# Optimization experiments

Measured on AMD Instinct MI355X. Metric: run time of the kernel, lower is better.

The kernel has to match this reference:

```python
import jax, jax.numpy as jnp
import numpy as np

B, S, D, H, DFF = 8, 1024, 1024, 16, 4096
DK = D // H
EPS = 1e-6
NEG = -1e9


def setup_inputs() -> dict:
    key = jax.random.key(0)
    ks = jax.random.split(key, 8)
    x = jax.random.normal(ks[0], (B, S, D), dtype=jnp.float32)
    mask = jnp.ones((B, 1, 1, S), dtype=jnp.int32)
    s = 0.02
    wq = jax.random.normal(ks[1], (D, D), jnp.float32) * s
    wk = jax.random.normal(ks[2], (D, D), jnp.float32) * s
    wv = jax.random.normal(ks[3], (D, D), jnp.float32) * s
    wo = jax.random.normal(ks[4], (D, D), jnp.float32) * s
    bq = jnp.zeros((D,), jnp.float32); bk = jnp.zeros((D,), jnp.float32)
    bv = jnp.zeros((D,), jnp.float32); bo = jnp.zeros((D,), jnp.float32)
    w1 = jax.random.normal(ks[5], (D, DFF), jnp.float32) * s
    b1 = jnp.zeros((DFF,), jnp.float32)
    w2 = jax.random.normal(ks[6], (DFF, D), jnp.float32) * s
    b2 = jnp.zeros((D,), jnp.float32)
    g1 = jnp.array(1.0, jnp.float32); be1 = jnp.array(0.0, jnp.float32)
    g2 = jnp.array(1.0, jnp.float32); be2 = jnp.array(0.0, jnp.float32)
    return dict(x=x, mask=mask, wq=wq, bq=bq, wk=wk, bk=bk, wv=wv, bv=bv,
                wo=wo, bo=bo, w1=w1, b1=b1, w2=w2, b2=b2,
                g1=g1, be1=be1, g2=g2, be2=be2)


def layer_norm(x, gamma, beta):
    # repo quirk: unbiased std (ddof=1), scalar gamma/beta, divide by (std+eps)
    mean = jnp.mean(x, axis=-1, keepdims=True)
    std = jnp.std(x, axis=-1, keepdims=True, ddof=1)
    return gamma * (x - mean) / (std + EPS) + beta


def mha(x, mask, wq, bq, wk, bk, wv, bv, wo, bo):
    q = (x @ wq + bq).reshape(B, S, H, DK).transpose(0, 2, 1, 3)  # bhsd
    k = (x @ wk + bk).reshape(B, S, H, DK).transpose(0, 2, 1, 3)
    v = (x @ wv + bv).reshape(B, S, H, DK).transpose(0, 2, 1, 3)
    scores = jnp.einsum('bhqd,bhkd->bhqk', q, k) / jnp.sqrt(jnp.float32(DK))
    scores = jnp.where(mask == 0, NEG, scores)
    attn = jax.nn.softmax(scores, axis=-1)
    out = jnp.einsum('bhqk,bhkd->bhqd', attn, v)
    out = out.transpose(0, 2, 1, 3).reshape(B, S, D)
    return out @ wo + bo


def reference(x, mask, wq, bq, wk, bk, wv, bv, wo, bo, w1, b1, w2, b2, g1, be1, g2, be2):
    # pre-LN residual: x + sublayer(norm(x)); dropout inert at eval
    x = x + mha(layer_norm(x, g1, be1), mask, wq, bq, wk, bk, wv, bv, wo, bo)
    h = layer_norm(x, g2, be2)
    x = x + (jax.nn.relu(h @ w1 + b1) @ w2 + b2)
    return x
```

## Files before the change

kernel.cpp:

```cpp
#include <hip/hip_runtime.h>
#include <math.h>

typedef __bf16 bf16;
typedef float f32x4 __attribute__((ext_vector_type(4)));
typedef bf16 bf16x8 __attribute__((ext_vector_type(8)));

#define DEV __device__ __forceinline__

constexpr int Ss = 1024, Dd = 1024;
constexpr float EPSf = 1e-6f;
constexpr float SM_SCALE = 0.125f * 1.4426950408889634f;

DEV void gl_lds16(const void* g, void* l) {
  __builtin_amdgcn_global_load_lds(
      (const __attribute__((address_space(1))) void*)g,
      (__attribute__((address_space(3))) void*)l, 16, 0, 0);
}

__global__ __launch_bounds__(256) void transpose6_k(
    const float* __restrict__ i0, const float* __restrict__ i1,
    const float* __restrict__ i2, const float* __restrict__ i3,
    const float* __restrict__ i4, const float* __restrict__ i5,
    bf16* __restrict__ o0, bf16* __restrict__ o1, bf16* __restrict__ o2,
    bf16* __restrict__ o3, bf16* __restrict__ o4, bf16* __restrict__ o5) {
  __shared__ float t[64 * 65];
  const int bi = blockIdx.x;
  const float* in;
  bf16* out;
  int R, C, local, sh;
  if (bi < 1024) {
    const int j = bi >> 8;
    local = bi & 255; R = 1024; C = 1024; sh = 4;
    in = (j == 0) ? i0 : (j == 1) ? i1 : (j == 2) ? i2 : i3;
    out = (j == 0) ? o0 : (j == 1) ? o1 : (j == 2) ? o2 : o3;
  } else if (bi < 2048) {
    local = bi - 1024; R = 1024; C = 4096; sh = 6; in = i4; out = o4;
  } else {
    local = bi - 2048; R = 4096; C = 1024; sh = 4; in = i5; out = o5;
  }
  const int nx = 1 << sh;
  const int bx = local & (nx - 1), by = local >> sh;
  const int tid = threadIdx.x;
  const int tx = tid & 63, ty = tid >> 6;
  const int r0 = by * 64, c0 = bx * 64;
#pragma unroll
  for (int i = 0; i < 16; i++) {
    int r = ty + i * 4;
    t[r * 65 + tx] = in[(size_t)(r0 + r) * C + c0 + tx];
  }
  __syncthreads();
#pragma unroll
  for (int i = 0; i < 16; i++) {
    int r = ty + i * 4;
    out[(size_t)(c0 + r) * R + r0 + tx] = (bf16)t[tx * 65 + r];
  }
}

__global__ __launch_bounds__(256) void transpose_b_k(
    const bf16* __restrict__ in, bf16* __restrict__ out, int ostride, int si,
    size_t isb, size_t osb) {
  __shared__ bf16 t[64 * 65];
  const int tid = threadIdx.x;
  const int tx = tid & 63, ty = tid >> 6;
  const bf16* ib = in + (size_t)blockIdx.z * isb;
  bf16* ob = out + (size_t)blockIdx.z * osb;
  const int r0 = blockIdx.y * 64, c0 = blockIdx.x * 64;
#pragma unroll
  for (int i = 0; i < 16; i++) {
    int r = ty + i * 4;
    t[r * 65 + tx] = ib[(size_t)(r0 + r) * si + c0 + tx];
  }
  __syncthreads();
#pragma unroll
  for (int i = 0; i < 16; i++) {
    int r = ty + i * 4;
    ob[(size_t)(c0 + r) * ostride + r0 + tx] = t[tx * 65 + r];
  }
}

__global__ __launch_bounds__(256) void ln_kernel(
    const float* __restrict__ in, bf16* __restrict__ out,
    const float* __restrict__ gp, const float* __restrict__ bp) {
  const int row = blockIdx.x;
  const int tid = threadIdx.x;
  float v[4];
  const float* p = in + (size_t)row * Dd + tid * 4;
#pragma unroll
  for (int i = 0; i < 4; i++) v[i] = p[i];
  float s = v[0] + v[1] + v[2] + v[3];
  float s2 = v[0] * v[0] + v[1] * v[1] + v[2] * v[2] + v[3] * v[3];
#pragma unroll
  for (int m = 1; m < 64; m <<= 1) {
    s += __shfl_xor(s, m, 64);
    s2 += __shfl_xor(s2, m, 64);
  }
  __shared__ float ls[4], ls2[4];
  if ((tid & 63) == 0) {
    ls[tid >> 6] = s;
    ls2[tid >> 6] = s2;
  }
  __syncthreads();
  s = ls[0] + ls[1] + ls[2] + ls[3];
  s2 = ls2[0] + ls2[1] + ls2[2] + ls2[3];
  float mean = s * (1.0f / Dd);
  float var = (s2 - (float)Dd * mean * mean) * (1.0f / (Dd - 1));
  var = fmaxf(var, 0.0f);
  float g = gp[0], be = bp[0];
  float rs = g / (sqrtf(var) + EPSf);
  bf16* q = out + (size_t)row * Dd + tid * 4;
#pragma unroll
  for (int i = 0; i < 4; i++) q[i] = (bf16)((v[i] - mean) * rs + be);
}

template <int EPI>
__global__ __launch_bounds__(256) void gemm_bt(
    const bf16* __restrict__ A, const bf16* __restrict__ Bt,
    const float* __restrict__ bias, const float* __restrict__ bias2,
    const float* __restrict__ bias3, const float* __restrict__ resid,
    void* __restrict__ Cout, int M, int N, int K, int sa, int sb) {
  __shared__ __attribute__((aligned(16))) bf16 As[128 * 64];
  __shared__ __attribute__((aligned(16))) bf16 Bs[128 * 64];
  const int tid = threadIdx.x;
  const int ln = tid & 63;
  const int wv = tid >> 6;
  const int wm = wv >> 1, wn = wv & 1;
  const int quad = ln >> 4, l16 = ln & 15;
  const int l7 = l16 & 7;
  const int m0 = blockIdx.y * 128, n0 = blockIdx.x * 128;

  f32x4 acc[4][4];
#pragma unroll
  for (int i = 0; i < 4; i++)
#pragma unroll
    for (int j = 0; j < 4; j++) acc[i][j] = {0.f, 0.f, 0.f, 0.f};

  const int sr = tid >> 3;
  const int sc = (tid & 7) ^ (sr & 7);
  const size_t abase = (size_t)(m0 + sr) * sa + sc * 8;
  const size_t bbase = (size_t)(n0 + sr) * sb + sc * 8;

  for (int k0 = 0; k0 < K; k0 += 64) {
#pragma unroll
    for (int j = 0; j < 4; j++) {
      gl_lds16(A + abase + (size_t)(j * 32) * sa + k0,
               (char*)As + j * 4096 + wv * 1024);
      gl_lds16(Bt + bbase + (size_t)(j * 32) * sb + k0,
               (char*)Bs + j * 4096 + wv * 1024);
    }
    __syncthreads();
#pragma unroll
    for (int kh = 0; kh < 2; kh++) {
      bf16x8 af[4], bfr[4];
#pragma unroll
      for (int mi = 0; mi < 4; mi++)
        af[mi] = *(const bf16x8*)&As[(wm * 64 + mi * 16 + l16) * 64 +
                                     ((kh * 4 + quad) ^ l7) * 8];
#pragma unroll
      for (int ni = 0; ni < 4; ni++)
        bfr[ni] = *(const bf16x8*)&Bs[(wn * 64 + ni * 16 + l16) * 64 +
                                      ((kh * 4 + quad) ^ l7) * 8];
#pragma unroll
      for (int mi = 0; mi < 4; mi++)
#pragma unroll
        for (int ni = 0; ni < 4; ni++)
          acc[mi][ni] = __builtin_amdgcn_mfma_f32_16x16x32_bf16(
              af[mi], bfr[ni], acc[mi][ni], 0, 0, 0);
    }
    __syncthreads();
  }

#pragma unroll
  for (int mi = 0; mi < 4; mi++) {
    const int m = m0 + wm * 64 + mi * 16 + quad * 4;
#pragma unroll
    for (int ni = 0; ni < 4; ni++) {
      const int n = n0 + wn * 64 + ni * 16 + l16;
      float bvl;
      if constexpr (EPI == 4) {
        const int seg = n >> 10;
        const float* bp = (seg == 0) ? bias : (seg == 1) ? bias2 : bias3;
        bvl = bp[n & 1023];
      } else if constexpr (EPI == 3) {
        bvl = 0.0f;
      } else {
        bvl = bias[n];
      }
#pragma unroll
      for (int r = 0; r < 4; r++) {
        float val = acc[mi][ni][r] + bvl;
        const size_t idx = (size_t)(m + r) * N + n;
        if constexpr (EPI == 1) {
          ((float*)Cout)[idx] = val + resid[idx];
        } else if constexpr (EPI == 2) {
          ((bf16*)Cout)[idx] = (bf16)fmaxf(val, 0.0f);
        } else if constexpr (EPI == 3) {
          ((float*)Cout)[idx] = val + resid[idx];
        } else {
          ((bf16*)Cout)[idx] = (bf16)val;
        }
      }
    }
  }
}

__global__ __launch_bounds__(256) void attn_k(
    const bf16* __restrict__ qkv, const bf16* __restrict__ vt,
    const int* __restrict__ mask, bf16* __restrict__ ctx) {
  __shared__ __attribute__((aligned(16))) bf16 Qs[128 * 64];
  __shared__ __attribute__((aligned(16))) bf16 Ks[64 * 64];
  __shared__ __attribute__((aligned(16))) bf16 Vs[64 * 64];
  __shared__ __attribute__((aligned(16))) bf16 Ps[4 * 32 * 64];
  __shared__ float Fm[1024];
  const int tid = threadIdx.x;
  const int ln = tid & 63, w = tid >> 6;
  const int quad = ln >> 4, l16 = ln & 15;
  const int l7 = l16 & 7;
  const int bh = blockIdx.y;
  const int b = bh >> 4, h = bh & 15;
  const int q0 = blockIdx.x * 128;
  const int sr = tid >> 3;
  const int sc = (tid & 7) ^ (sr & 7);

  {
    const int4 mv = *(const int4*)&mask[b * Ss + tid * 4];
    const float ninf = -__builtin_inff();
    Fm[tid * 4 + 0] = mv.x ? 0.0f : ninf;
    Fm[tid * 4 + 1] = mv.y ? 0.0f : ninf;
    Fm[tid * 4 + 2] = mv.z ? 0.0f : ninf;
    Fm[tid * 4 + 3] = mv.w ? 0.0f : ninf;
  }
  {
#pragma unroll
    for (int j = 0; j < 4; j++) {
      const size_t ga =
          (size_t)(b * Ss + q0 + j * 32 + sr) * 3072 + h * 64 + sc * 8;
      gl_lds16(qkv + ga, (char*)Qs + j * 4096 + w * 1024);
    }
  }
  __syncthreads();
  bf16x8 aq[2][2];
#pragma unroll
  for (int qi = 0; qi < 2; qi++)
#pragma unroll
    for (int c = 0; c < 2; c++)
      aq[qi][c] = *(const bf16x8*)&Qs[(w * 32 + qi * 16 + l16) * 64 +
                                      ((c * 4 + quad) ^ l7) * 8];

  f32x4 o[2][4];
#pragma unroll
  for (int qi = 0; qi < 2; qi++)
#pragma unroll
    for (int i = 0; i < 4; i++) o[qi][i] = {0.f, 0.f, 0.f, 0.f};
  f32x4 psum[2] = {{0.f, 0.f, 0.f, 0.f}, {0.f, 0.f, 0.f, 0.f}};

  for (int kk0 = 0; kk0 < Ss; kk0 += 64) {
    {
#pragma unroll
      for (int j = 0; j < 2; j++) {
        const size_t ga = (size_t)(b * Ss + kk0 + j * 32 + sr) * 3072 + 1024 +
                          h * 64 + sc * 8;
        gl_lds16(qkv + ga, (char*)Ks + j * 4096 + w * 1024);
        const size_t gv = (size_t)(bh * 64 + j * 32 + sr) * Ss + kk0 + sc * 8;
        gl_lds16(vt + gv, (char*)Vs + j * 4096 + w * 1024);
      }
    }
    __syncthreads();

    f32x4 st[2][4];
#pragma unroll
    for (int nt = 0; nt < 4; nt++) {
      bf16x8 bk0 = *(const bf16x8*)&Ks[(nt * 16 + l16) * 64 + (quad ^ l7) * 8];
      bf16x8 bk1 =
          *(const bf16x8*)&Ks[(nt * 16 + l16) * 64 + ((4 + quad) ^ l7) * 8];
#pragma unroll
      for (int qi = 0; qi < 2; qi++) {
        f32x4 s = {0.f, 0.f, 0.f, 0.f};
        s = __builtin_amdgcn_mfma_f32_16x16x32_bf16(aq[qi][0], bk0, s, 0, 0, 0);
        s = __builtin_amdgcn_mfma_f32_16x16x32_bf16(aq[qi][1], bk1, s, 0, 0, 0);
        st[qi][nt] = s;
      }
    }
    float fmv[4];
#pragma unroll
    for (int nt = 0; nt < 4; nt++) fmv[nt] = Fm[kk0 + nt * 16 + l16];
#pragma unroll
    for (int qi = 0; qi < 2; qi++)
#pragma unroll
      for (int nt = 0; nt < 4; nt++)
#pragma unroll
        for (int r = 0; r < 4; r++) {
          const float p = exp2f(fmaf(st[qi][nt][r], SM_SCALE, fmv[nt]));
          st[qi][nt][r] = p;
          psum[qi][r] += p;
        }
#pragma unroll
    for (int qi = 0; qi < 2; qi++)
#pragma unroll
      for (int nt = 0; nt < 4; nt++) {
        const int ch = nt * 2 + (l16 >> 3);
#pragma unroll
        for (int r = 0; r < 4; r++) {
          const int pr = qi * 16 + quad * 4 + r;
          Ps[w * 2048 + pr * 64 + (ch ^ (pr & 7)) * 8 + l7] =
              (bf16)st[qi][nt][r];
        }
      }
#pragma unroll
    for (int kh = 0; kh < 2; kh++) {
      bf16x8 bv[4];
#pragma unroll
      for (int dt = 0; dt < 4; dt++)
        bv[dt] = *(const bf16x8*)&Vs[(dt * 16 + l16) * 64 +
                                     ((kh * 4 + quad) ^ l7) * 8];
#pragma unroll
      for (int qi = 0; qi < 2; qi++) {
        bf16x8 ap = *(const bf16x8*)&Ps[w * 2048 + (qi * 16 + l16) * 64 +
                                        ((kh * 4 + quad) ^ l7) * 8];
#pragma unroll
        for (int dt = 0; dt < 4; dt++)
          o[qi][dt] =
              __builtin_amdgcn_mfma_f32_16x16x32_bf16(ap, bv[dt], o[qi][dt],
                                                      0, 0, 0);
      }
    }
    __syncthreads();
  }
#pragma unroll
  for (int qi = 0; qi < 2; qi++)
#pragma unroll
    for (int r = 0; r < 4; r++) {
      float s = psum[qi][r];
#pragma unroll
      for (int m = 1; m < 16; m <<= 1) s += __shfl_xor(s, m, 64);
      psum[qi][r] = s;
    }
#pragma unroll
  for (int qi = 0; qi < 2; qi++) {
    const float inv0 = 1.0f / psum[qi][0], inv1 = 1.0f / psum[qi][1];
    const float inv2 = 1.0f / psum[qi][2], inv3 = 1.0f / psum[qi][3];
#pragma unroll
    for (int dt = 0; dt < 4; dt++) {
      const size_t base =
          (size_t)(b * Ss + q0 + w * 32 + qi * 16 + quad * 4) * Dd + h * 64 +
          dt * 16 + l16;
      ctx[base] = (bf16)(o[qi][dt][0] * inv0);
      ctx[base + Dd] = (bf16)(o[qi][dt][1] * inv1);
      ctx[base + 2 * Dd] = (bf16)(o[qi][dt][2] * inv2);
      ctx[base + 3 * Dd] = (bf16)(o[qi][dt][3] * inv3);
    }
  }
}

extern "C" void kernel_launch(void* const* d_in, const int* in_sizes, int n_in,
                              void* d_out, int out_size, void* d_ws,
                              size_t ws_size, hipStream_t stream) {
  (void)in_sizes; (void)n_in; (void)out_size;
  const float* x = (const float*)d_in[0];
  const int* mask = (const int*)d_in[1];
  const float* wq = (const float*)d_in[2];
  const float* bq = (const float*)d_in[3];
  const float* wk = (const float*)d_in[4];
  const float* bk = (const float*)d_in[5];
  const float* wvw = (const float*)d_in[6];
  const float* bv = (const float*)d_in[7];
  const float* wo = (const float*)d_in[8];
  const float* bo = (const float*)d_in[9];
  const float* w1 = (const float*)d_in[10];
  const float* b1 = (const float*)d_in[11];
  const float* w2 = (const float*)d_in[12];
  const float* b2 = (const float*)d_in[13];
  const float* g1 = (const float*)d_in[14];
  const float* be1 = (const float*)d_in[15];
  const float* g2 = (const float*)d_in[16];
  const float* be2 = (const float*)d_in[17];
  float* out = (float*)d_out;

  char* ws = (char*)d_ws;
  const size_t MB = 1024 * 1024;
  bf16* w1T = (bf16*)(ws + 0 * MB);
  bf16* w2T = (bf16*)(ws + 8 * MB);
  bf16* wqkvT = (bf16*)(ws + 16 * MB);
  bf16* woT = (bf16*)(ws + 22 * MB);
  bf16* lnb = (bf16*)(ws + 24 * MB);
  bf16* qkv = (bf16*)(ws + 40 * MB);
  bf16* vtb = (bf16*)(ws + 88 * MB);
  float* x1 = (float*)(ws + 40 * MB);
  bf16* ctx = lnb;

  dim3 blk(256);
  transpose6_k<<<3072, blk, 0, stream>>>(
      wq, wk, wvw, wo, w1, w2, wqkvT, wqkvT + (size_t)1024 * 1024,
      wqkvT + (size_t)2048 * 1024, woT, w1T, w2T);
  ln_kernel<<<8192, blk, 0, stream>>>(x, lnb, g1, be1);
  gemm_bt<4><<<dim3(24, 64), blk, 0, stream>>>(
      lnb, wqkvT, bq, bk, bv, nullptr, qkv, 8192, 3072, 1024, 1024, 1024);
  transpose_b_k<<<dim3(16, 16, 8), blk, 0, stream>>>(
      qkv + 2048, vtb, 1024, 3072, (size_t)Ss * 3072, (size_t)Dd * Ss);
  attn_k<<<dim3(8, 128), blk, 0, stream>>>(qkv, vtb, mask, ctx);
  gemm_bt<1><<<dim3(8, 64), blk, 0, stream>>>(
      ctx, woT, bo, nullptr, nullptr, x, x1, 8192, 1024, 1024, 1024, 1024);
  ln_kernel<<<8192, blk, 0, stream>>>(x1, lnb, g2, be2);

  if (ws_size >= 136 * MB) {
    bf16* mid = (bf16*)(ws + 72 * MB);
    gemm_bt<2><<<dim3(32, 64), blk, 0, stream>>>(
        lnb, w1T, b1, nullptr, nullptr, nullptr, mid, 8192, 4096, 1024, 1024,
        1024);
    gemm_bt<1><<<dim3(8, 64), blk, 0, stream>>>(
        mid, w2T, b2, nullptr, nullptr, x1, out, 8192, 1024, 4096, 4096, 4096);
  } else {
    bf16* mid = (bf16*)(ws + 72 * MB);
    gemm_bt<2><<<dim3(16, 64), blk, 0, stream>>>(
        lnb, w1T, b1, nullptr, nullptr, nullptr, mid, 8192, 2048, 1024, 1024,
        1024);
    gemm_bt<1><<<dim3(8, 64), blk, 0, stream>>>(
        mid, w2T, b2, nullptr, nullptr, x1, out, 8192, 1024, 2048, 2048, 4096);
    gemm_bt<2><<<dim3(16, 64), blk, 0, stream>>>(
        lnb, w1T + (size_t)2048 * 1024, b1 + 2048, nullptr, nullptr, nullptr,
        mid, 8192, 2048, 1024, 1024, 1024);
    gemm_bt<3><<<dim3(8, 64), blk, 0, stream>>>(
        mid, w2T + 2048, nullptr, nullptr, nullptr, out, out, 8192, 1024, 2048,
        2048, 4096);
  }
}
```

Baseline: 511.2 us.

## Fuse V transpose into QKV GEMM epilogue and deepen K tile for N=1024 GEMMs

The QKV projection epilogue now writes the V third directly in transposed layout into the vtb buffer, removing the separate transpose kernel and its extra read/write of V. The GEMM is templated on the K tile size, and the output-projection and FFN-down GEMMs use a 128-wide K tile to halve loop iterations and barriers. The larger tile doubles LDS use per block, which may reduce occupancy, and the transposed V stores are narrow scattered 8-byte writes.

```diff
diff --git a/kernel.cpp b/kernel.cpp
--- a/kernel.cpp
+++ b/kernel.cpp
@@ -4,6 +4,7 @@
 typedef __bf16 bf16;
 typedef float f32x4 __attribute__((ext_vector_type(4)));
 typedef bf16 bf16x8 __attribute__((ext_vector_type(8)));
+typedef bf16 bf16x4 __attribute__((ext_vector_type(4)));
 
 #define DEV __device__ __forceinline__
 
@@ -56,28 +57,6 @@
   }
 }
 
-__global__ __launch_bounds__(256) void transpose_b_k(
-    const bf16* __restrict__ in, bf16* __restrict__ out, int ostride, int si,
-    size_t isb, size_t osb) {
-  __shared__ bf16 t[64 * 65];
-  const int tid = threadIdx.x;
-  const int tx = tid & 63, ty = tid >> 6;
-  const bf16* ib = in + (size_t)blockIdx.z * isb;
-  bf16* ob = out + (size_t)blockIdx.z * osb;
-  const int r0 = blockIdx.y * 64, c0 = blockIdx.x * 64;
-#pragma unroll
-  for (int i = 0; i < 16; i++) {
-    int r = ty + i * 4;
-    t[r * 65 + tx] = ib[(size_t)(r0 + r) * si + c0 + tx];
-  }
-  __syncthreads();
-#pragma unroll
-  for (int i = 0; i < 16; i++) {
-    int r = ty + i * 4;
-    ob[(size_t)(c0 + r) * ostride + r0 + tx] = t[tx * 65 + r];
-  }
-}
-
 __global__ __launch_bounds__(256) void ln_kernel(
     const float* __restrict__ in, bf16* __restrict__ out,
     const float* __restrict__ gp, const float* __restrict__ bp) {
@@ -112,14 +91,18 @@
   for (int i = 0; i < 4; i++) q[i] = (bf16)((v[i] - mean) * rs + be);
 }
 
-template <int EPI>
+template <int EPI, int BK>
 __global__ __launch_bounds__(256) void gemm_bt(
     const bf16* __restrict__ A, const bf16* __restrict__ Bt,
     const float* __restrict__ bias, const float* __restrict__ bias2,
     const float* __restrict__ bias3, const float* __restrict__ resid,
-    void* __restrict__ Cout, int M, int N, int K, int sa, int sb) {
-  __shared__ __attribute__((aligned(16))) bf16 As[128 * 64];
-  __shared__ __attribute__((aligned(16))) bf16 Bs[128 * 64];
+    bf16* __restrict__ vtb, void* __restrict__ Cout, int M, int N, int K,
+    int sa, int sb) {
+  __shared__ __attribute__((aligned(16))) bf16 As[128 * BK];
+  __shared__ __attribute__((aligned(16))) bf16 Bs[128 * BK];
+  constexpr int CPR = BK / 8;
+  constexpr int RPJ = 256 / CPR;
+  constexpr int NJ = BK / 16;
   const int tid = threadIdx.x;
   const int ln = tid & 63;
   const int wv = tid >> 6;
@@ -134,30 +117,30 @@
 #pragma unroll
     for (int j = 0; j < 4; j++) acc[i][j] = {0.f, 0.f, 0.f, 0.f};
 
-  const int sr = tid >> 3;
-  const int sc = (tid & 7) ^ (sr & 7);
+  const int sr = tid / CPR;
+  const int sc = (tid & (CPR - 1)) ^ (sr & 7);
   const size_t abase = (size_t)(m0 + sr) * sa + sc * 8;
   const size_t bbase = (size_t)(n0 + sr) * sb + sc * 8;
 
-  for (int k0 = 0; k0 < K; k0 += 64) {
-#pragma unroll
-    for (int j = 0; j < 4; j++) {
-      gl_lds16(A + abase + (size_t)(j * 32) * sa + k0,
+  for (int k0 = 0; k0 < K; k0 += BK) {
+#pragma unroll
+    for (int j = 0; j < NJ; j++) {
+      gl_lds16(A + abase + (size_t)(j * RPJ) * sa + k0,
                (char*)As + j * 4096 + wv * 1024);
-      gl_lds16(Bt + bbase + (size_t)(j * 32) * sb + k0,
+      gl_lds16(Bt + bbase + (size_t)(j * RPJ) * sb + k0,
                (char*)Bs + j * 4096 + wv * 1024);
     }
     __syncthreads();
 #pragma unroll
-    for (int kh = 0; kh < 2; kh++) {
+    for (int kh = 0; kh < BK / 32; kh++) {
       bf16x8 af[4], bfr[4];
 #pragma unroll
       for (int mi = 0; mi < 4; mi++)
-        af[mi] = *(const bf16x8*)&As[(wm * 64 + mi * 16 + l16) * 64 +
+        af[mi] = *(const bf16x8*)&As[(wm * 64 + mi * 16 + l16) * BK +
                                      ((kh * 4 + quad) ^ l7) * 8];
 #pragma unroll
       for (int ni = 0; ni < 4; ni++)
-        bfr[ni] = *(const bf16x8*)&Bs[(wn * 64 + ni * 16 + l16) * 64 +
+        bfr[ni] = *(const bf16x8*)&Bs[(wn * 64 + ni * 16 + l16) * BK +
                                       ((kh * 4 + quad) ^ l7) * 8];
 #pragma unroll
       for (int mi = 0; mi < 4; mi++)
@@ -185,18 +168,31 @@
       } else {
         bvl = bias[n];
       }
-#pragma unroll
-      for (int r = 0; r < 4; r++) {
-        float val = acc[mi][ni][r] + bvl;
-        const size_t idx = (size_t)(m + r) * N + n;
-        if constexpr (EPI == 1) {
-          ((float*)Cout)[idx] = val + resid[idx];
-        } else if constexpr (EPI == 2) {
-          ((bf16*)Cout)[idx] = (bf16)fmaxf(val, 0.0f);
-        } else if constexpr (EPI == 3) {
-          ((float*)Cout)[idx] = val + resid[idx];
+      if constexpr (EPI == 4) {
+        if (n < 2048) {
+#pragma unroll
+          for (int r = 0; r < 4; r++)
+            ((bf16*)Cout)[(size_t)(m + r) * N + n] =
+                (bf16)(acc[mi][ni][r] + bvl);
         } else {
-          ((bf16*)Cout)[idx] = (bf16)val;
+          bf16x4 tv;
+#pragma unroll
+          for (int r = 0; r < 4; r++) tv[r] = (bf16)(acc[mi][ni][r] + bvl);
+          const size_t vrow = (size_t)((m >> 10) * 1024 + (n - 2048));
+          *(bf16x4*)&vtb[vrow * Ss + (m & 1023)] = tv;
+        }
+      } else {
+#pragma unroll
+        for (int r = 0; r < 4; r++) {
+          float val = acc[mi][ni][r] + bvl;
+          const size_t idx = (size_t)(m + r) * N + n;
+          if constexpr (EPI == 1) {
+            ((float*)Cout)[idx] = val + resid[idx];
+          } else if constexpr (EPI == 2) {
+            ((bf16*)Cout)[idx] = (bf16)fmaxf(val, 0.0f);
+          } else {
+            ((float*)Cout)[idx] = val + resid[idx];
+          }
         }
       }
     }
@@ -392,34 +388,35 @@
       wq, wk, wvw, wo, w1, w2, wqkvT, wqkvT + (size_t)1024 * 1024,
       wqkvT + (size_t)2048 * 1024, woT, w1T, w2T);
   ln_kernel<<<8192, blk, 0, stream>>>(x, lnb, g1, be1);
-  gemm_bt<4><<<dim3(24, 64), blk, 0, stream>>>(
-      lnb, wqkvT, bq, bk, bv, nullptr, qkv, 8192, 3072, 1024, 1024, 1024);
-  transpose_b_k<<<dim3(16, 16, 8), blk, 0, stream>>>(
-      qkv + 2048, vtb, 1024, 3072, (size_t)Ss * 3072, (size_t)Dd * Ss);
+  gemm_bt<4, 64><<<dim3(24, 64), blk, 0, stream>>>(
+      lnb, wqkvT, bq, bk, bv, nullptr, vtb, qkv, 8192, 3072, 1024, 1024, 1024);
   attn_k<<<dim3(8, 128), blk, 0, stream>>>(qkv, vtb, mask, ctx);
-  gemm_bt<1><<<dim3(8, 64), blk, 0, stream>>>(
-      ctx, woT, bo, nullptr, nullptr, x, x1, 8192, 1024, 1024, 1024, 1024);
+  gemm_bt<1, 128><<<dim3(8, 64), blk, 0, stream>>>(
+      ctx, woT, bo, nullptr, nullptr, x, nullptr, x1, 8192, 1024, 1024, 1024,
+      1024);
   ln_kernel<<<8192, blk, 0, stream>>>(x1, lnb, g2, be2);
 
   if (ws_size >= 136 * MB) {
     bf16* mid = (bf16*)(ws + 72 * MB);
-    gemm_bt<2><<<dim3(32, 64), blk, 0, stream>>>(
-        lnb, w1T, b1, nullptr, nullptr, nullptr, mid, 8192, 4096, 1024, 1024,
-        1024);
-    gemm_bt<1><<<dim3(8, 64), blk, 0, stream>>>(
-        mid, w2T, b2, nullptr, nullptr, x1, out, 8192, 1024, 4096, 4096, 4096);
+    gemm_bt<2, 64><<<dim3(32, 64), blk, 0, stream>>>(
+        lnb, w1T, b1, nullptr, nullptr, nullptr, nullptr, mid, 8192, 4096,
+        1024, 1024, 1024);
+    gemm_bt<1, 128><<<dim3(8, 64), blk, 0, stream>>>(
+        mid, w2T, b2, nullptr, nullptr, x1, nullptr, out, 8192, 1024, 4096,
+        4096, 4096);
   } else {
     bf16* mid = (bf16*)(ws + 72 * MB);
-    gemm_bt<2><<<dim3(16, 64), blk, 0, stream>>>(
-        lnb, w1T, b1, nullptr, nullptr, nullptr, mid, 8192, 2048, 1024, 1024,
-        1024);
-    gemm_bt<1><<<dim3(8, 64), blk, 0, stream>>>(
-        mid, w2T, b2, nullptr, nullptr, x1, out, 8192, 1024, 2048, 2048, 4096);
-    gemm_bt<2><<<dim3(16, 64), blk, 0, stream>>>(
+    gemm_bt<2, 64><<<dim3(16, 64), blk, 0, stream>>>(
+        lnb, w1T, b1, nullptr, nullptr, nullptr, nullptr, mid, 8192, 2048,
+        1024, 1024, 1024);
+    gemm_bt<1, 128><<<dim3(8, 64), blk, 0, stream>>>(
+        mid, w2T, b2, nullptr, nullptr, x1, nullptr, out, 8192, 1024, 2048,
+        2048, 4096);
+    gemm_bt<2, 64><<<dim3(16, 64), blk, 0, stream>>>(
         lnb, w1T + (size_t)2048 * 1024, b1 + 2048, nullptr, nullptr, nullptr,
-        mid, 8192, 2048, 1024, 1024, 1024);
-    gemm_bt<3><<<dim3(8, 64), blk, 0, stream>>>(
-        mid, w2T + 2048, nullptr, nullptr, nullptr, out, out, 8192, 1024, 2048,
-        2048, 4096);
-  }
-}
+        nullptr, mid, 8192, 2048, 1024, 1024, 1024);
+    gemm_bt<3, 128><<<dim3(8, 64), blk, 0, stream>>>(
+        mid, w2T + 2048, nullptr, nullptr, nullptr, out, nullptr, out, 8192,
+        1024, 2048, 2048, 4096);
+  }
+}
```

Result: no change. 510.5 us (-0.1%).
